# Kernel tuning notes

Hardware: AMD Instinct MI355X
Metric: run time of the kernel (lower is better)

Reference implementation:

```python
import jax, jax.numpy as jnp
import numpy as np

B, T, D = 2, 2048, 1024
H, HD = 16, 32
INNER = H * HD
FF = 4 * D
KT, KP = 3, 15


def _layernorm(x, g, b, eps=1e-5):
    mu = jnp.mean(x, axis=-1, keepdims=True)
    var = jnp.var(x, axis=-1, keepdims=True)
    return (x - mu) * jax.lax.rsqrt(var + eps) * g + b


def _causal_dwconv(x, w, b):
    # x: (b,t,d), w: (d,1,k) depthwise kernel; causal left-pad of k-1
    k = w.shape[-1]
    xc = jnp.transpose(x, (0, 2, 1))  # (b,d,t)
    xp = jnp.pad(xc, ((0, 0), (0, 0), (k - 1, 0)))
    y = jax.lax.conv_general_dilated(
        xp, w, window_strides=(1,), padding='VALID',
        feature_group_count=x.shape[-1],
        dimension_numbers=('NCH', 'OIH', 'NCH'))
    return jnp.transpose(y + b[None, :, None], (0, 2, 1))


def _causal_linear_attention(q, k, v, mask):
    # q,k,v: (b,t,h,d); mask: (b,t)
    m = mask[:, :, None, None]
    q = (jax.nn.elu(q) + 1.0) * m
    k = (jax.nn.elu(k) + 1.0) * m
    v = v * m
    kv = jnp.einsum('bthd,bthe->bthde', k, v)
    kv_prefix = jnp.cumsum(kv, axis=1)          # (b,t,h,d,e) large intermediate
    k_prefix = jnp.cumsum(k, axis=1)
    num = jnp.einsum('bthd,bthde->bthe', q, kv_prefix)
    den = jnp.sum(q * k_prefix, axis=-1, keepdims=True)
    return (num / (den + 1e-6)) * m


def setup_inputs() -> dict:
    key = jax.random.key(0)
    ks = jax.random.split(key, 10)
    w = lambda i, shape: jax.random.normal(ks[i], shape, jnp.float32) * 0.02
    return {
        'inputs': jax.random.normal(ks[0], (B, T, D), jnp.float32),
        'mask': jnp.ones((B, T), jnp.float32),
        'ln1_g': jnp.ones((D,), jnp.float32), 'ln1_b': jnp.zeros((D,), jnp.float32),
        'W_in': w(1, (D, D + 3 * INNER)), 'b_in': jnp.zeros((D + 3 * INNER,), jnp.float32),
        'W_c': w(2, (INNER, D)), 'b_c': jnp.zeros((D,), jnp.float32),
        'w_t': w(3, (D, 1, KT)), 'b_t': jnp.zeros((D,), jnp.float32),
        'w_p': w(4, (D, 1, KP)), 'b_p': jnp.zeros((D,), jnp.float32),
        'W_mix': w(5, (3 * D, D)), 'b_mix': jnp.zeros((D,), jnp.float32),
        'ln2_g': jnp.ones((D,), jnp.float32), 'ln2_b': jnp.zeros((D,), jnp.float32),
        'W1': w(6, (D, FF)), 'b1': jnp.zeros((FF,), jnp.float32),
        'W2': w(7, (FF, D)), 'b2': jnp.zeros((D,), jnp.float32),
    }


def reference(inputs, mask, ln1_g, ln1_b, W_in, b_in, W_c, b_c, w_t, b_t,
              w_p, b_p, W_mix, b_mix, ln2_g, ln2_b, W1, b1, W2, b2):
    residual = inputs
    normed = _layernorm(inputs, ln1_g, ln1_b)
    proj = normed @ W_in + b_in
    gate, q, k, v = jnp.split(proj, [D, D + INNER, D + 2 * INNER], axis=-1)
    b, t, _ = inputs.shape
    q = q.reshape(b, t, H, HD)
    k = k.reshape(b, t, H, HD)
    v = v.reshape(b, t, H, HD)
    content = _causal_linear_attention(q, k, v, mask).reshape(b, t, INNER)
    content = content @ W_c + b_c
    temporal = _causal_dwconv(normed, w_t, b_t)
    positional = _causal_dwconv(normed, w_p, b_p)
    mixed = jnp.concatenate((content, temporal, positional), axis=-1) @ W_mix + b_mix
    mask_f = mask[:, :, None]
    out = residual + jax.nn.sigmoid(gate) * mixed  # dropout=0.0 -> identity
    out = out * mask_f
    h = _layernorm(out, ln2_g, ln2_b)
    ffn = jax.nn.gelu(h @ W1 + b1, approximate=False) @ W2 + b2
    out = out + ffn
    return out * mask_f
```

## Files before the change

### kernel.cpp

```cpp
#include <hip/hip_runtime.h>
#include <math.h>

#define BB 2
#define TT 2048
#define DD 1024
#define HH 16
#define INNERD 512
#define FFD 4096
#define NPROJ 2560
#define CATD 3072
#define MROWS (BB*TT)
#define CHUNK 64
#define NCH (TT/CHUNK)
#define BH 32

typedef __bf16 bf16;
typedef __attribute__((ext_vector_type(8))) __bf16 bf16x8;
typedef __attribute__((ext_vector_type(4))) __bf16 bf16x4;
typedef __attribute__((ext_vector_type(4))) float f32x4;

struct Part4 { void* p0; void* p1; void* p2; void* p3; };

__global__ __launch_bounds__(256) void layernorm_k(
    const float* __restrict__ x, const float* __restrict__ g,
    const float* __restrict__ bta, bf16* __restrict__ y)
{
    int row = blockIdx.x, tid = threadIdx.x;
    f32x4 xv = ((const f32x4*)(x + (size_t)row * DD))[tid];
    float s = xv[0] + xv[1] + xv[2] + xv[3];
    float s2 = xv[0]*xv[0] + xv[1]*xv[1] + xv[2]*xv[2] + xv[3]*xv[3];
    #pragma unroll
    for (int off = 32; off > 0; off >>= 1) {
        s  += __shfl_xor(s,  off, 64);
        s2 += __shfl_xor(s2, off, 64);
    }
    __shared__ float rs[4], rs2[4];
    int wid = tid >> 6;
    if ((tid & 63) == 0) { rs[wid] = s; rs2[wid] = s2; }
    __syncthreads();
    s  = rs[0] + rs[1] + rs[2] + rs[3];
    s2 = rs2[0] + rs2[1] + rs2[2] + rs2[3];
    float mean = s * (1.0f / DD);
    float var  = s2 * (1.0f / DD) - mean * mean;
    float rstd = rsqrtf(var + 1e-5f);
    f32x4 gv = ((const f32x4*)g)[tid];
    f32x4 bv = ((const f32x4*)bta)[tid];
    bf16x4 o;
    #pragma unroll
    for (int q = 0; q < 4; q++)
        o[q] = (bf16)((xv[q] - mean) * rstd * gv[q] + bv[q]);
    ((bf16x4*)(y + (size_t)row * DD))[tid] = o;
}

__global__ __launch_bounds__(256) void transpose_cvt(
    const float* __restrict__ W, bf16* __restrict__ Wt, int Kd, int Nd)
{
    __shared__ float t[32][33];
    int nb = blockIdx.x * 32, kb = blockIdx.y * 32;
    int tx = threadIdx.x & 31, ty = threadIdx.x >> 5;
    #pragma unroll
    for (int r = 0; r < 32; r += 8)
        t[ty + r][tx] = W[(size_t)(kb + ty + r) * Nd + nb + tx];
    __syncthreads();
    #pragma unroll
    for (int r = 0; r < 32; r += 8)
        Wt[(size_t)(nb + ty + r) * Kd + kb + tx] = (bf16)t[tx][ty + r];
}

template<int EPI>
__global__ __launch_bounds__(256, 4) void gemm_mfma(
    const bf16* __restrict__ A,  int lda,
    const bf16* __restrict__ Bt, int ldb,
    const float* __restrict__ bias,
    bf16* __restrict__ Cb, int ldc,
    int K, Part4 part)
{
    __shared__ bf16 As[128 * 64];
    __shared__ bf16 Bs[128 * 64];
    const int tid  = threadIdx.x;
    const int wave = tid >> 6, lane = tid & 63;
    const int m0 = blockIdx.y * 128, n0 = blockIdx.x * 128;
    const int koff = blockIdx.z * K;
    A  += koff;
    Bt += koff;
    const int wr = wave >> 1, wc = wave & 1;
    const int lrow = lane >> 2;
    const int lcol = (lane & 3) * 8;
    const int fm = lane & 15;
    const int fk = (lane >> 4) * 8;

    f32x4 acc[4][4];
    #pragma unroll
    for (int i = 0; i < 4; i++)
        #pragma unroll
        for (int j = 0; j < 4; j++)
            acc[i][j] = (f32x4){0.f, 0.f, 0.f, 0.f};

    for (int k0 = 0; k0 < K; k0 += 64) {
        #pragma unroll
        for (int r = 0; r < 4; r++) {
            int c  = r * 4 + wave;
            int rc = c >> 1, kh = c & 1;
            const bf16* ga = A  + (size_t)(m0 + rc * 16 + lrow) * lda + k0 + kh * 32 + lcol;
            const bf16* gb = Bt + (size_t)(n0 + rc * 16 + lrow) * ldb + k0 + kh * 32 + lcol;
            __builtin_amdgcn_global_load_lds(
                (const __attribute__((address_space(1))) void*)ga,
                (__attribute__((address_space(3))) void*)(As + c * 512), 16, 0, 0);
            __builtin_amdgcn_global_load_lds(
                (const __attribute__((address_space(1))) void*)gb,
                (__attribute__((address_space(3))) void*)(Bs + c * 512), 16, 0, 0);
        }
        __syncthreads();
        #pragma unroll
        for (int ks = 0; ks < 2; ks++) {
            bf16x8 af[4], bfv[4];
            #pragma unroll
            for (int i = 0; i < 4; i++)
                af[i] = *(const bf16x8*)(As + (wr * 4 + i) * 1024 + ks * 512 + fm * 32 + fk);
            #pragma unroll
            for (int j = 0; j < 4; j++)
                bfv[j] = *(const bf16x8*)(Bs + (wc * 4 + j) * 1024 + ks * 512 + fm * 32 + fk);
            #pragma unroll
            for (int i = 0; i < 4; i++)
                #pragma unroll
                for (int j = 0; j < 4; j++)
                    acc[i][j] = __builtin_amdgcn_mfma_f32_16x16x32_bf16(
                        af[i], bfv[j], acc[i][j], 0, 0, 0);
        }
        __syncthreads();
    }

    void* psel = nullptr;
    if constexpr (EPI == 4 || EPI == 5) {
        int z = blockIdx.z;
        psel = (z == 0) ? part.p0 : (z == 1) ? part.p1 : (z == 2) ? part.p2 : part.p3;
    }

    #pragma unroll
    for (int i = 0; i < 4; i++) {
        int mbase = m0 + wr * 64 + i * 16 + (lane >> 4) * 4;
        #pragma unroll
        for (int j = 0; j < 4; j++) {
            int col = n0 + wc * 64 + j * 16 + (lane & 15);
            float bv = 0.f;
            if constexpr (EPI == 0 || EPI == 1) bv = bias[col];
            #pragma unroll
            for (int r = 0; r < 4; r++) {
                int row = mbase + r;
                float v = acc[i][j][r] + bv;
                if constexpr (EPI == 0) {
                    Cb[(size_t)row * ldc + col] = (bf16)v;
                } else if constexpr (EPI == 1) {
                    float z2 = v * (1.5957691f + 0.07135502f * v * v);
                    v = v / (1.0f + __expf(-z2));
                    Cb[(size_t)row * ldc + col] = (bf16)v;
                } else if constexpr (EPI == 4) {
                    ((bf16*)psel)[(size_t)row * DD + col] = (bf16)v;
                } else {
                    ((float*)psel)[(size_t)row * DD + col] = v;
                }
            }
        }
    }
}

__global__ __launch_bounds__(256) void epi_wc(
    const float* __restrict__ P0, const float* __restrict__ P1,
    const float* __restrict__ bias, bf16* __restrict__ cat)
{
    int id = blockIdx.x * 256 + threadIdx.x;
    int row = id >> 8, cg = id & 255;
    f32x4 s0 = ((const f32x4*)P0)[id];
    f32x4 s1 = ((const f32x4*)P1)[id];
    f32x4 b  = ((const f32x4*)bias)[cg];
    bf16x4 o;
    #pragma unroll
    for (int q = 0; q < 4; q++) o[q] = (bf16)(s0[q] + s1[q] + b[q]);
    *(bf16x4*)(cat + (size_t)row * CATD + cg * 4) = o;
}

__global__ __launch_bounds__(256) void epi_mix_ln2(
    const bf16* __restrict__ P0, const bf16* __restrict__ P1,
    const bf16* __restrict__ P2, const float* __restrict__ bias,
    const bf16* __restrict__ proj, const float* __restrict__ res,
    const float* __restrict__ mask,
    const float* __restrict__ g2, const float* __restrict__ b2v,
    float* __restrict__ out1, bf16* __restrict__ hbuf)
{
    int row = blockIdx.x, tid = threadIdx.x;
    float m = mask[row];
    size_t off = (size_t)row * DD + tid * 4;
    bf16x4 s0 = *(const bf16x4*)(P0 + off);
    bf16x4 s1 = *(const bf16x4*)(P1 + off);
    bf16x4 s2v = *(const bf16x4*)(P2 + off);
    f32x4 bv = ((const f32x4*)bias)[tid];
    bf16x4 g4 = *(const bf16x4*)(proj + (size_t)row * NPROJ + tid * 4);
    f32x4 rv = ((const f32x4*)(res + (size_t)row * DD))[tid];
    f32x4 v;
    #pragma unroll
    for (int q = 0; q < 4; q++) {
        float sg = 1.0f / (1.0f + __expf(-(float)g4[q]));
        float sv = (float)s0[q] + (float)s1[q] + (float)s2v[q] + bv[q];
        v[q] = (rv[q] + sg * sv) * m;
    }
    ((f32x4*)(out1 + (size_t)row * DD))[tid] = v;
    float s = v[0] + v[1] + v[2] + v[3];
    float s2 = v[0]*v[0] + v[1]*v[1] + v[2]*v[2] + v[3]*v[3];
    #pragma unroll
    for (int off2 = 32; off2 > 0; off2 >>= 1) {
        s  += __shfl_xor(s,  off2, 64);
        s2 += __shfl_xor(s2, off2, 64);
    }
    __shared__ float rs[4], rs2[4];
    int wid = tid >> 6;
    if ((tid & 63) == 0) { rs[wid] = s; rs2[wid] = s2; }
    __syncthreads();
    s  = rs[0] + rs[1] + rs[2] + rs[3];
    s2 = rs2[0] + rs2[1] + rs2[2] + rs2[3];
    float mean = s * (1.0f / DD);
    float var  = s2 * (1.0f / DD) - mean * mean;
    float rstd = rsqrtf(var + 1e-5f);
    f32x4 gg = ((const f32x4*)g2)[tid];
    f32x4 bb = ((const f32x4*)b2v)[tid];
    bf16x4 h;
    #pragma unroll
    for (int q = 0; q < 4; q++)
        h[q] = (bf16)((v[q] - mean) * rstd * gg[q] + bb[q]);
    ((bf16x4*)(hbuf + (size_t)row * DD))[tid] = h;
}

__global__ __launch_bounds__(256) void epi_w2(
    float* __restrict__ d_out, const float* __restrict__ out1,
    const bf16* __restrict__ P0, const bf16* __restrict__ P1,
    const bf16* __restrict__ P2, const bf16* __restrict__ P3,
    const float* __restrict__ bias, const float* __restrict__ mask)
{
    int id = blockIdx.x * 256 + threadIdx.x;
    int row = id >> 8;
    float m = mask[row];
    bf16x4 a0 = ((const bf16x4*)P0)[id];
    bf16x4 a1 = ((const bf16x4*)P1)[id];
    bf16x4 a2 = ((const bf16x4*)P2)[id];
    bf16x4 a3 = ((const bf16x4*)P3)[id];
    f32x4 r = ((const f32x4*)out1)[id];
    f32x4 b = ((const f32x4*)bias)[id & 255];
    f32x4 o;
    #pragma unroll
    for (int q = 0; q < 4; q++) {
        float sv = (float)a0[q] + (float)a1[q] + (float)a2[q] + (float)a3[q];
        o[q] = (r[q] + sv + b[q]) * m;
    }
    ((f32x4*)d_out)[id] = o;
}

__global__ __launch_bounds__(256) void dwconv_fused(
    const bf16* __restrict__ x,
    const float* __restrict__ w_t, const float* __restrict__ b_t,
    const float* __restrict__ w_p, const float* __restrict__ b_p,
    bf16* __restrict__ cat)
{
    int id = blockIdx.x * 256 + threadIdx.x;
    int cg = id & 127, rp = id >> 7;
    int c0 = cg * 8;
    int row0 = rp * 2;
    int t0 = row0 & (TT - 1);
    bf16x8 xw[16];
    #pragma unroll
    for (int j = 0; j < 16; j++) {
        int t = t0 - 14 + j;
        if (t >= 0)
            xw[j] = *(const bf16x8*)(x + (size_t)(row0 - 14 + j) * DD + c0);
        else
            #pragma unroll
            for (int q = 0; q < 8; q++) xw[j][q] = (bf16)0.f;
    }
    float y15[2][8], y3[2][8];
    #pragma unroll
    for (int q = 0; q < 8; q++) {
        float bp = b_p[c0 + q], bt = b_t[c0 + q];
        y15[0][q] = bp; y15[1][q] = bp;
        y3[0][q] = bt;  y3[1][q] = bt;
    }
    #pragma unroll
    for (int i = 0; i < 15; i++) {
        float wp[8];
        #pragma unroll
        for (int q = 0; q < 8; q++) wp[q] = w_p[(c0 + q) * 15 + i];
        #pragma unroll
        for (int rr = 0; rr < 2; rr++)
            #pragma unroll
            for (int q = 0; q < 8; q++)
                y15[rr][q] = fmaf(wp[q], (float)xw[rr + i][q], y15[rr][q]);
    }
    #pragma unroll
    for (int i = 0; i < 3; i++) {
        float wt[8];
        #pragma unroll
        for (int q = 0; q < 8; q++) wt[q] = w_t[(c0 + q) * 3 + i];
        #pragma unroll
        for (int rr = 0; rr < 2; rr++)
            #pragma unroll
            for (int q = 0; q < 8; q++)
                y3[rr][q] = fmaf(wt[q], (float)xw[rr + 12 + i][q], y3[rr][q]);
    }
    #pragma unroll
    for (int rr = 0; rr < 2; rr++) {
        bf16x8 o3, o15;
        #pragma unroll
        for (int q = 0; q < 8; q++) { o3[q] = (bf16)y3[rr][q]; o15[q] = (bf16)y15[rr][q]; }
        *(bf16x8*)(cat + (size_t)(row0 + rr) * CATD + DD + c0)     = o3;
        *(bf16x8*)(cat + (size_t)(row0 + rr) * CATD + 2 * DD + c0) = o15;
    }
}

__device__ __forceinline__ float phi_f(float x) {
    return x > 0.f ? x + 1.f : __expf(x);
}

__global__ __launch_bounds__(64) void attn_sums(
    const bf16* __restrict__ proj, const float* __restrict__ mask,
    float* __restrict__ kvsum, float* __restrict__ kssum)
{
    int blk = blockIdx.x;
    int c  = blk & (NCH - 1);
    int bh = blk >> 5;
    int b  = bh >> 4, hh = bh & (HH - 1);
    int lane = threadIdx.x;
    __shared__ float ks[CHUNK][32], vs[CHUNK][32];
    int row0 = b * TT + c * CHUNK;
    {
        int row = row0 + lane;
        float m = mask[row];
        const bf16* kp = proj + (size_t)row * NPROJ + DD + INNERD + hh * 32;
        const bf16* vp = kp + INNERD;
        #pragma unroll
        for (int s = 0; s < 4; s++) {
            bf16x8 k8 = *(const bf16x8*)(kp + s * 8);
            bf16x8 v8 = *(const bf16x8*)(vp + s * 8);
            #pragma unroll
            for (int q = 0; q < 8; q++) {
                ks[lane][s * 8 + q] = phi_f((float)k8[q]) * m;
                vs[lane][s * 8 + q] = (float)v8[q] * m;
            }
        }
    }
    __syncthreads();
    int e = lane & 31, d0 = (lane >> 5) * 16;
    float kv[16], ksl[16];
    #pragma unroll
    for (int j = 0; j < 16; j++) { kv[j] = 0.f; ksl[j] = 0.f; }
    for (int t = 0; t < CHUNK; t++) {
        float ve = vs[t][e];
        f32x4 kr[4];
        #pragma unroll
        for (int s = 0; s < 4; s++) kr[s] = *(const f32x4*)&ks[t][d0 + s * 4];
        #pragma unroll
        for (int j = 0; j < 16; j++) {
            float kval = kr[j >> 2][j & 3];
            kv[j] = fmaf(kval, ve, kv[j]);
            ksl[j] += kval;
        }
    }
    size_t base = (size_t)blk * 1024;
    #pragma unroll
    for (int j = 0; j < 16; j++)
        kvsum[base + (size_t)(d0 + j) * 32 + e] = kv[j];
    if (e == 0) {
        #pragma unroll
        for (int j = 0; j < 16; j++)
            kssum[blk * 32 + d0 + j] = ksl[j];
    }
}

__global__ __launch_bounds__(256) void attn_prefix(
    const float* __restrict__ kvsum, const float* __restrict__ kssum,
    float* __restrict__ kvpref, float* __restrict__ kspref)
{
    int bh = blockIdx.x;
    int tid = threadIdx.x;
    float run[4] = {0.f, 0.f, 0.f, 0.f};
    for (int c = 0; c < NCH; c++) {
        size_t base = (size_t)(bh * NCH + c) * 1024 + tid * 4;
        #pragma unroll
        for (int q = 0; q < 4; q++) {
            kvpref[base + q] = run[q];
            run[q] += kvsum[base + q];
        }
    }
    if (tid < 32) {
        float r = 0.f;
        for (int c = 0; c < NCH; c++) {
            kspref[(bh * NCH + c) * 32 + tid] = r;
            r += kssum[(bh * NCH + c) * 32 + tid];
        }
    }
}

__global__ __launch_bounds__(64) void attn_scan(
    const bf16* __restrict__ proj, const float* __restrict__ mask,
    const float* __restrict__ kvpref, const float* __restrict__ kspref,
    bf16* __restrict__ attn_out)
{
    int blk = blockIdx.x;
    int c  = blk & (NCH - 1);
    int bh = blk >> 5;
    int b  = bh >> 4, hh = bh & (HH - 1);
    int lane = threadIdx.x;
    __shared__ float qs[CHUNK][32], ks[CHUNK][32], vs[CHUNK][32];
    __shared__ float ms[CHUNK];
    int row0 = b * TT + c * CHUNK;
    {
        int row = row0 + lane;
        float m = mask[row];
        ms[lane] = m;
        const bf16* qp = proj + (size_t)row * NPROJ + DD + hh * 32;
        const bf16* kp = qp + INNERD;
        const bf16* vp = kp + INNERD;
        #pragma unroll
        for (int s = 0; s < 4; s++) {
            bf16x8 q8 = *(const bf16x8*)(qp + s * 8);
            bf16x8 k8 = *(const bf16x8*)(kp + s * 8);
            bf16x8 v8 = *(const bf16x8*)(vp + s * 8);
            #pragma unroll
            for (int q = 0; q < 8; q++) {
                qs[lane][s * 8 + q] = phi_f((float)q8[q]) * m;
                ks[lane][s * 8 + q] = phi_f((float)k8[q]) * m;
                vs[lane][s * 8 + q] = (float)v8[q] * m;
            }
        }
    }
    int e = lane & 31, d0 = (lane >> 5) * 16;
    float kv[16], ksl[16];
    size_t base = (size_t)blk * 1024;
    #pragma unroll
    for (int j = 0; j < 16; j++) kv[j] = kvpref[base + (size_t)(d0 + j) * 32 + e];
    #pragma unroll
    for (int j = 0; j < 16; j++) ksl[j] = kspref[blk * 32 + d0 + j];
    __syncthreads();
    for (int t = 0; t < CHUNK; t++) {
        float ve = vs[t][e];
        f32x4 kr[4], qr[4];
        #pragma unroll
        for (int s = 0; s < 4; s++) kr[s] = *(const f32x4*)&ks[t][d0 + s * 4];
        #pragma unroll
        for (int s = 0; s < 4; s++) qr[s] = *(const f32x4*)&qs[t][d0 + s * 4];
        float num0 = 0.f, num1 = 0.f, den0 = 0.f, den1 = 0.f;
        #pragma unroll
        for (int j = 0; j < 16; j++) {
            float kval = kr[j >> 2][j & 3], qval = qr[j >> 2][j & 3];
            kv[j]  = fmaf(kval, ve, kv[j]);
            ksl[j] += kval;
            if (j & 1) { num1 = fmaf(qval, kv[j], num1); den1 = fmaf(qval, ksl[j], den1); }
            else       { num0 = fmaf(qval, kv[j], num0); den0 = fmaf(qval, ksl[j], den0); }
        }
        float num = num0 + num1, den = den0 + den1;
        num += __shfl_xor(num, 32, 64);
        den += __shfl_xor(den, 32, 64);
        if (lane < 32)
            attn_out[(size_t)(row0 + t) * INNERD + hh * 32 + e] =
                (bf16)(num / (den + 1e-6f) * ms[t]);
    }
}

extern "C" void kernel_launch(void* const* d_in, const int* in_sizes, int n_in,
                              void* d_out, int out_size, void* d_ws, size_t ws_size,
                              hipStream_t stream)
{
    const float* inputs = (const float*)d_in[0];
    const float* mask   = (const float*)d_in[1];
    const float* ln1_g  = (const float*)d_in[2];
    const float* ln1_b  = (const float*)d_in[3];
    const float* W_in   = (const float*)d_in[4];
    const float* b_in   = (const float*)d_in[5];
    const float* W_c    = (const float*)d_in[6];
    const float* b_c    = (const float*)d_in[7];
    const float* w_t    = (const float*)d_in[8];
    const float* b_t    = (const float*)d_in[9];
    const float* w_p    = (const float*)d_in[10];
    const float* b_p    = (const float*)d_in[11];
    const float* W_mix  = (const float*)d_in[12];
    const float* b_mix  = (const float*)d_in[13];
    const float* ln2_g  = (const float*)d_in[14];
    const float* ln2_b  = (const float*)d_in[15];
    const float* W1     = (const float*)d_in[16];
    const float* b1     = (const float*)d_in[17];
    const float* W2     = (const float*)d_in[18];
    const float* b2     = (const float*)d_in[19];
    float* out = (float*)d_out;

    char* p = (char*)d_ws;
    bf16* normed = (bf16*)p;  p += (size_t)MROWS * DD * 2;
    bf16* proj   = (bf16*)p;  p += (size_t)MROWS * NPROJ * 2;
    bf16* attnb  = (bf16*)p;  p += (size_t)MROWS * INNERD * 2;
    bf16* cat    = (bf16*)p;  p += (size_t)MROWS * CATD * 2;
    float* out1  = (float*)p; p += (size_t)MROWS * DD * 4;
    bf16* hbuf   = (bf16*)p;  p += (size_t)MROWS * DD * 2;
    bf16* wt_in  = (bf16*)p;  p += (size_t)NPROJ * DD * 2;
    bf16* wt_c   = (bf16*)p;  p += (size_t)DD * INNERD * 2;
    bf16* wt_mix = (bf16*)p;  p += (size_t)DD * CATD * 2;
    bf16* wt1    = (bf16*)p;  p += (size_t)FFD * DD * 2;
    bf16* wt2    = (bf16*)p;  p += (size_t)DD * FFD * 2;
    bf16* ffn1   = (bf16*)d_ws;
    float* kvsum = out1;
    float* kvpref= kvsum  + (size_t)BH * NCH * 1024;
    float* kssum = kvpref + (size_t)BH * NCH * 1024;
    float* kspref= kssum  + (size_t)BH * NCH * 32;
    float* c_p0  = (float*)d_out;
    float* c_p1  = out1;
    bf16*  m_p0  = (bf16*)d_out;
    bf16*  m_p1  = (bf16*)d_out + (size_t)MROWS * DD;
    bf16*  m_p2  = hbuf;
    bf16*  w2_p0 = cat;
    bf16*  w2_p1 = cat + (size_t)MROWS * DD;
    bf16*  w2_p2 = cat + (size_t)MROWS * DD * 2;
    bf16*  w2_p3 = hbuf;

    transpose_cvt<<<dim3(NPROJ/32, DD/32),   256, 0, stream>>>(W_in,  wt_in,  DD,     NPROJ);
    transpose_cvt<<<dim3(DD/32,    INNERD/32),256, 0, stream>>>(W_c,   wt_c,   INNERD, DD);
    transpose_cvt<<<dim3(DD/32,    CATD/32), 256, 0, stream>>>(W_mix, wt_mix, CATD,   DD);
    transpose_cvt<<<dim3(FFD/32,   DD/32),   256, 0, stream>>>(W1,    wt1,    DD,     FFD);
    transpose_cvt<<<dim3(DD/32,    FFD/32),  256, 0, stream>>>(W2,    wt2,    FFD,    DD);

    layernorm_k<<<MROWS, 256, 0, stream>>>(inputs, ln1_g, ln1_b, normed);
    gemm_mfma<0><<<dim3(NPROJ/128, MROWS/128), 256, 0, stream>>>(
        normed, DD, wt_in, DD, b_in, proj, NPROJ, DD, Part4{});
    attn_sums  <<<BH * NCH, 64, 0, stream>>>(proj, mask, kvsum, kssum);
    attn_prefix<<<BH, 256, 0, stream>>>(kvsum, kssum, kvpref, kspref);
    attn_scan  <<<BH * NCH, 64, 0, stream>>>(proj, mask, kvpref, kspref, attnb);
    dwconv_fused<<<(MROWS/2) * 128 / 256, 256, 0, stream>>>(normed, w_t, b_t, w_p, b_p, cat);
    gemm_mfma<5><<<dim3(DD/128, MROWS/128, 2), 256, 0, stream>>>(
        attnb, INNERD, wt_c, INNERD, nullptr, nullptr, DD, INNERD / 2,
        Part4{c_p0, c_p1, nullptr, nullptr});
    epi_wc<<<MROWS * DD / 4 / 256, 256, 0, stream>>>(c_p0, c_p1, b_c, cat);
    gemm_mfma<4><<<dim3(DD/128, MROWS/128, 3), 256, 0, stream>>>(
        cat, CATD, wt_mix, CATD, nullptr, nullptr, DD, CATD / 3,
        Part4{m_p0, m_p1, m_p2, nullptr});
    epi_mix_ln2<<<MROWS, 256, 0, stream>>>(m_p0, m_p1, m_p2, b_mix, proj, inputs,
                                           mask, ln2_g, ln2_b, out1, hbuf);
    gemm_mfma<1><<<dim3(FFD/128, MROWS/128), 256, 0, stream>>>(
        hbuf, DD, wt1, DD, b1, ffn1, FFD, DD, Part4{});
    gemm_mfma<4><<<dim3(DD/128, MROWS/128, 4), 256, 0, stream>>>(
        ffn1, FFD, wt2, FFD, nullptr, nullptr, DD, FFD / 4,
        Part4{w2_p0, w2_p1, w2_p2, w2_p3});
    epi_w2<<<MROWS * DD / 4 / 256, 256, 0, stream>>>(out, out1, w2_p0, w2_p1,
                                                     w2_p2, w2_p3, b2, mask);
}
```

Baseline: 426.2 us.

## Fuse prep and mid kernels, swap GEMM grid order, store W_c partials in bf16

Merges layernorm and the five weight transpose/convert launches into one prep kernel, and merges the depthwise convs with the attention chunk-sum stage into one mid kernel that packs two attention chunks per 256-thread block. It also swaps the GEMM grid so blockIdx.x walks M tiles instead of N tiles, changing tile scheduling order and cache reuse. The split-K partials of the W_c GEMM are now written as bf16 instead of fp32, which halves that traffic but adds rounding error. The intent is fewer launches and less memory traffic. In the mid kernel, half the threads of each attention block exit immediately, and the shared-memory sync in the attention stage was removed on the assumption that each wave owns its own buffers.

```diff
diff --git a/kernel.cpp b/kernel.cpp
--- a/kernel.cpp
+++ b/kernel.cpp
@@ -21,43 +21,55 @@
 
 struct Part4 { void* p0; void* p1; void* p2; void* p3; };
 
-__global__ __launch_bounds__(256) void layernorm_k(
-    const float* __restrict__ x, const float* __restrict__ g,
-    const float* __restrict__ bta, bf16* __restrict__ y)
-{
-    int row = blockIdx.x, tid = threadIdx.x;
-    f32x4 xv = ((const f32x4*)(x + (size_t)row * DD))[tid];
-    float s = xv[0] + xv[1] + xv[2] + xv[3];
-    float s2 = xv[0]*xv[0] + xv[1]*xv[1] + xv[2]*xv[2] + xv[3]*xv[3];
-    #pragma unroll
-    for (int off = 32; off > 0; off >>= 1) {
-        s  += __shfl_xor(s,  off, 64);
-        s2 += __shfl_xor(s2, off, 64);
-    }
-    __shared__ float rs[4], rs2[4];
-    int wid = tid >> 6;
-    if ((tid & 63) == 0) { rs[wid] = s; rs2[wid] = s2; }
-    __syncthreads();
-    s  = rs[0] + rs[1] + rs[2] + rs[3];
-    s2 = rs2[0] + rs2[1] + rs2[2] + rs2[3];
-    float mean = s * (1.0f / DD);
-    float var  = s2 * (1.0f / DD) - mean * mean;
-    float rstd = rsqrtf(var + 1e-5f);
-    f32x4 gv = ((const f32x4*)g)[tid];
-    f32x4 bv = ((const f32x4*)bta)[tid];
-    bf16x4 o;
-    #pragma unroll
-    for (int q = 0; q < 4; q++)
-        o[q] = (bf16)((xv[q] - mean) * rstd * gv[q] + bv[q]);
-    ((bf16x4*)(y + (size_t)row * DD))[tid] = o;
-}
-
-__global__ __launch_bounds__(256) void transpose_cvt(
-    const float* __restrict__ W, bf16* __restrict__ Wt, int Kd, int Nd)
-{
+__global__ __launch_bounds__(256) void prep_fused(
+    const float* __restrict__ inputs, const float* __restrict__ ln1_g,
+    const float* __restrict__ ln1_b, bf16* __restrict__ normed,
+    const float* __restrict__ W_in,  bf16* __restrict__ wt_in,
+    const float* __restrict__ W_c,   bf16* __restrict__ wt_c,
+    const float* __restrict__ W_mix, bf16* __restrict__ wt_mix,
+    const float* __restrict__ W1,    bf16* __restrict__ wt1,
+    const float* __restrict__ W2,    bf16* __restrict__ wt2)
+{
+    int blk = blockIdx.x, tid = threadIdx.x;
+    if (blk < MROWS) {
+        int row = blk;
+        f32x4 xv = ((const f32x4*)(inputs + (size_t)row * DD))[tid];
+        float s = xv[0] + xv[1] + xv[2] + xv[3];
+        float s2 = xv[0]*xv[0] + xv[1]*xv[1] + xv[2]*xv[2] + xv[3]*xv[3];
+        #pragma unroll
+        for (int off = 32; off > 0; off >>= 1) {
+            s  += __shfl_xor(s,  off, 64);
+            s2 += __shfl_xor(s2, off, 64);
+        }
+        __shared__ float rs[4], rs2[4];
+        int wid = tid >> 6;
+        if ((tid & 63) == 0) { rs[wid] = s; rs2[wid] = s2; }
+        __syncthreads();
+        s  = rs[0] + rs[1] + rs[2] + rs[3];
+        s2 = rs2[0] + rs2[1] + rs2[2] + rs2[3];
+        float mean = s * (1.0f / DD);
+        float var  = s2 * (1.0f / DD) - mean * mean;
+        float rstd = rsqrtf(var + 1e-5f);
+        f32x4 gv = ((const f32x4*)ln1_g)[tid];
+        f32x4 bv = ((const f32x4*)ln1_b)[tid];
+        bf16x4 o;
+        #pragma unroll
+        for (int q = 0; q < 4; q++)
+            o[q] = (bf16)((xv[q] - mean) * rstd * gv[q] + bv[q]);
+        ((bf16x4*)(normed + (size_t)row * DD))[tid] = o;
+        return;
+    }
+    int tb = blk - MROWS;
+    const float* W; bf16* Wt; int Kd, Nd;
+    if      (tb < 2560)  {             W = W_in;  Wt = wt_in;  Kd = 1024; Nd = 2560; }
+    else if (tb < 3072)  { tb -= 2560; W = W_c;   Wt = wt_c;   Kd = 512;  Nd = 1024; }
+    else if (tb < 6144)  { tb -= 3072; W = W_mix; Wt = wt_mix; Kd = 3072; Nd = 1024; }
+    else if (tb < 10240) { tb -= 6144; W = W1;    Wt = wt1;    Kd = 1024; Nd = 4096; }
+    else                 { tb -= 10240;W = W2;    Wt = wt2;    Kd = 4096; Nd = 1024; }
+    int ntx = Nd >> 5;
+    int nb = (tb % ntx) * 32, kb = (tb / ntx) * 32;
     __shared__ float t[32][33];
-    int nb = blockIdx.x * 32, kb = blockIdx.y * 32;
-    int tx = threadIdx.x & 31, ty = threadIdx.x >> 5;
+    int tx = tid & 31, ty = tid >> 5;
     #pragma unroll
     for (int r = 0; r < 32; r += 8)
         t[ty + r][tx] = W[(size_t)(kb + ty + r) * Nd + nb + tx];
@@ -79,7 +91,7 @@
     __shared__ bf16 Bs[128 * 64];
     const int tid  = threadIdx.x;
     const int wave = tid >> 6, lane = tid & 63;
-    const int m0 = blockIdx.y * 128, n0 = blockIdx.x * 128;
+    const int m0 = blockIdx.x * 128, n0 = blockIdx.y * 128;
     const int koff = blockIdx.z * K;
     A  += koff;
     Bt += koff;
@@ -131,7 +143,7 @@
     }
 
     void* psel = nullptr;
-    if constexpr (EPI == 4 || EPI == 5) {
+    if constexpr (EPI == 4) {
         int z = blockIdx.z;
         psel = (z == 0) ? part.p0 : (z == 1) ? part.p1 : (z == 2) ? part.p2 : part.p3;
     }
@@ -154,10 +166,8 @@
                     float z2 = v * (1.5957691f + 0.07135502f * v * v);
                     v = v / (1.0f + __expf(-z2));
                     Cb[(size_t)row * ldc + col] = (bf16)v;
-                } else if constexpr (EPI == 4) {
+                } else {
                     ((bf16*)psel)[(size_t)row * DD + col] = (bf16)v;
-                } else {
-                    ((float*)psel)[(size_t)row * DD + col] = v;
                 }
             }
         }
@@ -165,17 +175,17 @@
 }
 
 __global__ __launch_bounds__(256) void epi_wc(
-    const float* __restrict__ P0, const float* __restrict__ P1,
+    const bf16* __restrict__ P0, const bf16* __restrict__ P1,
     const float* __restrict__ bias, bf16* __restrict__ cat)
 {
     int id = blockIdx.x * 256 + threadIdx.x;
     int row = id >> 8, cg = id & 255;
-    f32x4 s0 = ((const f32x4*)P0)[id];
-    f32x4 s1 = ((const f32x4*)P1)[id];
+    bf16x4 s0 = ((const bf16x4*)P0)[id];
+    bf16x4 s1 = ((const bf16x4*)P1)[id];
     f32x4 b  = ((const f32x4*)bias)[cg];
     bf16x4 o;
     #pragma unroll
-    for (int q = 0; q < 4; q++) o[q] = (bf16)(s0[q] + s1[q] + b[q]);
+    for (int q = 0; q < 4; q++) o[q] = (bf16)((float)s0[q] + (float)s1[q] + b[q]);
     *(bf16x4*)(cat + (size_t)row * CATD + cg * 4) = o;
 }
 
@@ -253,80 +263,84 @@
     ((f32x4*)d_out)[id] = o;
 }
 
-__global__ __launch_bounds__(256) void dwconv_fused(
+__device__ __forceinline__ float phi_f(float x) {
+    return x > 0.f ? x + 1.f : __expf(x);
+}
+
+__global__ __launch_bounds__(256) void mid_fused(
     const bf16* __restrict__ x,
     const float* __restrict__ w_t, const float* __restrict__ b_t,
     const float* __restrict__ w_p, const float* __restrict__ b_p,
-    bf16* __restrict__ cat)
-{
-    int id = blockIdx.x * 256 + threadIdx.x;
-    int cg = id & 127, rp = id >> 7;
-    int c0 = cg * 8;
-    int row0 = rp * 2;
-    int t0 = row0 & (TT - 1);
-    bf16x8 xw[16];
-    #pragma unroll
-    for (int j = 0; j < 16; j++) {
-        int t = t0 - 14 + j;
-        if (t >= 0)
-            xw[j] = *(const bf16x8*)(x + (size_t)(row0 - 14 + j) * DD + c0);
-        else
-            #pragma unroll
-            for (int q = 0; q < 8; q++) xw[j][q] = (bf16)0.f;
-    }
-    float y15[2][8], y3[2][8];
-    #pragma unroll
-    for (int q = 0; q < 8; q++) {
-        float bp = b_p[c0 + q], bt = b_t[c0 + q];
-        y15[0][q] = bp; y15[1][q] = bp;
-        y3[0][q] = bt;  y3[1][q] = bt;
-    }
-    #pragma unroll
-    for (int i = 0; i < 15; i++) {
-        float wp[8];
-        #pragma unroll
-        for (int q = 0; q < 8; q++) wp[q] = w_p[(c0 + q) * 15 + i];
-        #pragma unroll
-        for (int rr = 0; rr < 2; rr++)
-            #pragma unroll
-            for (int q = 0; q < 8; q++)
-                y15[rr][q] = fmaf(wp[q], (float)xw[rr + i][q], y15[rr][q]);
-    }
-    #pragma unroll
-    for (int i = 0; i < 3; i++) {
-        float wt[8];
-        #pragma unroll
-        for (int q = 0; q < 8; q++) wt[q] = w_t[(c0 + q) * 3 + i];
-        #pragma unroll
-        for (int rr = 0; rr < 2; rr++)
-            #pragma unroll
-            for (int q = 0; q < 8; q++)
-                y3[rr][q] = fmaf(wt[q], (float)xw[rr + 12 + i][q], y3[rr][q]);
-    }
-    #pragma unroll
-    for (int rr = 0; rr < 2; rr++) {
-        bf16x8 o3, o15;
-        #pragma unroll
-        for (int q = 0; q < 8; q++) { o3[q] = (bf16)y3[rr][q]; o15[q] = (bf16)y15[rr][q]; }
-        *(bf16x8*)(cat + (size_t)(row0 + rr) * CATD + DD + c0)     = o3;
-        *(bf16x8*)(cat + (size_t)(row0 + rr) * CATD + 2 * DD + c0) = o15;
-    }
-}
-
-__device__ __forceinline__ float phi_f(float x) {
-    return x > 0.f ? x + 1.f : __expf(x);
-}
-
-__global__ __launch_bounds__(64) void attn_sums(
+    bf16* __restrict__ cat,
     const bf16* __restrict__ proj, const float* __restrict__ mask,
     float* __restrict__ kvsum, float* __restrict__ kssum)
 {
-    int blk = blockIdx.x;
-    int c  = blk & (NCH - 1);
-    int bh = blk >> 5;
+    __shared__ float s_ks[2][CHUNK][32], s_vs[2][CHUNK][32];
+    int blk = blockIdx.x, tid = threadIdx.x;
+    if (blk < 1024) {
+        int id = blk * 256 + tid;
+        int cg = id & 127, rp = id >> 7;
+        int c0 = cg * 8;
+        int row0 = rp * 2;
+        int t0 = row0 & (TT - 1);
+        bf16x8 xw[16];
+        #pragma unroll
+        for (int j = 0; j < 16; j++) {
+            int t = t0 - 14 + j;
+            if (t >= 0)
+                xw[j] = *(const bf16x8*)(x + (size_t)(row0 - 14 + j) * DD + c0);
+            else
+                #pragma unroll
+                for (int q = 0; q < 8; q++) xw[j][q] = (bf16)0.f;
+        }
+        float y15[2][8], y3[2][8];
+        #pragma unroll
+        for (int q = 0; q < 8; q++) {
+            float bp = b_p[c0 + q], bt = b_t[c0 + q];
+            y15[0][q] = bp; y15[1][q] = bp;
+            y3[0][q] = bt;  y3[1][q] = bt;
+        }
+        #pragma unroll
+        for (int i = 0; i < 15; i++) {
+            float wp[8];
+            #pragma unroll
+            for (int q = 0; q < 8; q++) wp[q] = w_p[(c0 + q) * 15 + i];
+            #pragma unroll
+            for (int rr = 0; rr < 2; rr++)
+                #pragma unroll
+                for (int q = 0; q < 8; q++)
+                    y15[rr][q] = fmaf(wp[q], (float)xw[rr + i][q], y15[rr][q]);
+        }
+        #pragma unroll
+        for (int i = 0; i < 3; i++) {
+            float wt[8];
+            #pragma unroll
+            for (int q = 0; q < 8; q++) wt[q] = w_t[(c0 + q) * 3 + i];
+            #pragma unroll
+            for (int rr = 0; rr < 2; rr++)
+                #pragma unroll
+                for (int q = 0; q < 8; q++)
+                    y3[rr][q] = fmaf(wt[q], (float)xw[rr + 12 + i][q], y3[rr][q]);
+        }
+        #pragma unroll
+        for (int rr = 0; rr < 2; rr++) {
+            bf16x8 o3, o15;
+            #pragma unroll
+            for (int q = 0; q < 8; q++) { o3[q] = (bf16)y3[rr][q]; o15[q] = (bf16)y15[rr][q]; }
+            *(bf16x8*)(cat + (size_t)(row0 + rr) * CATD + DD + c0)     = o3;
+            *(bf16x8*)(cat + (size_t)(row0 + rr) * CATD + 2 * DD + c0) = o15;
+        }
+        return;
+    }
+    int w = tid >> 6;
+    if (w >= 2) return;
+    int lane = tid & 63;
+    int ci = (blk - 1024) * 2 + w;
+    int c  = ci & (NCH - 1);
+    int bh = ci >> 5;
     int b  = bh >> 4, hh = bh & (HH - 1);
-    int lane = threadIdx.x;
-    __shared__ float ks[CHUNK][32], vs[CHUNK][32];
+    float (*ks)[32] = s_ks[w];
+    float (*vs)[32] = s_vs[w];
     int row0 = b * TT + c * CHUNK;
     {
         int row = row0 + lane;
@@ -344,7 +358,6 @@
             }
         }
     }
-    __syncthreads();
     int e = lane & 31, d0 = (lane >> 5) * 16;
     float kv[16], ksl[16];
     #pragma unroll
@@ -361,14 +374,14 @@
             ksl[j] += kval;
         }
     }
-    size_t base = (size_t)blk * 1024;
+    size_t base = (size_t)ci * 1024;
     #pragma unroll
     for (int j = 0; j < 16; j++)
         kvsum[base + (size_t)(d0 + j) * 32 + e] = kv[j];
     if (e == 0) {
         #pragma unroll
         for (int j = 0; j < 16; j++)
-            kssum[blk * 32 + d0 + j] = ksl[j];
+            kssum[ci * 32 + d0 + j] = ksl[j];
     }
 }
 
@@ -505,8 +518,8 @@
     float* kvpref= kvsum  + (size_t)BH * NCH * 1024;
     float* kssum = kvpref + (size_t)BH * NCH * 1024;
     float* kspref= kssum  + (size_t)BH * NCH * 32;
-    float* c_p0  = (float*)d_out;
-    float* c_p1  = out1;
+    bf16*  c_p0  = (bf16*)d_out;
+    bf16*  c_p1  = (bf16*)out1;
     bf16*  m_p0  = (bf16*)d_out;
     bf16*  m_p1  = (bf16*)d_out + (size_t)MROWS * DD;
     bf16*  m_p2  = hbuf;
@@ -515,31 +528,27 @@
     bf16*  w2_p2 = cat + (size_t)MROWS * DD * 2;
     bf16*  w2_p3 = hbuf;
 
-    transpose_cvt<<<dim3(NPROJ/32, DD/32),   256, 0, stream>>>(W_in,  wt_in,  DD,     NPROJ);
-    transpose_cvt<<<dim3(DD/32,    INNERD/32),256, 0, stream>>>(W_c,   wt_c,   INNERD, DD);
-    transpose_cvt<<<dim3(DD/32,    CATD/32), 256, 0, stream>>>(W_mix, wt_mix, CATD,   DD);
-    transpose_cvt<<<dim3(FFD/32,   DD/32),   256, 0, stream>>>(W1,    wt1,    DD,     FFD);
-    transpose_cvt<<<dim3(DD/32,    FFD/32),  256, 0, stream>>>(W2,    wt2,    FFD,    DD);
-
-    layernorm_k<<<MROWS, 256, 0, stream>>>(inputs, ln1_g, ln1_b, normed);
-    gemm_mfma<0><<<dim3(NPROJ/128, MROWS/128), 256, 0, stream>>>(
+    prep_fused<<<MROWS + 14336, 256, 0, stream>>>(
+        inputs, ln1_g, ln1_b, normed,
+        W_in, wt_in, W_c, wt_c, W_mix, wt_mix, W1, wt1, W2, wt2);
+    gemm_mfma<0><<<dim3(MROWS/128, NPROJ/128), 256, 0, stream>>>(
         normed, DD, wt_in, DD, b_in, proj, NPROJ, DD, Part4{});
-    attn_sums  <<<BH * NCH, 64, 0, stream>>>(proj, mask, kvsum, kssum);
+    mid_fused<<<1024 + 512, 256, 0, stream>>>(
+        normed, w_t, b_t, w_p, b_p, cat, proj, mask, kvsum, kssum);
     attn_prefix<<<BH, 256, 0, stream>>>(kvsum, kssum, kvpref, kspref);
     attn_scan  <<<BH * NCH, 64, 0, stream>>>(proj, mask, kvpref, kspref, attnb);
-    dwconv_fused<<<(MROWS/2) * 128 / 256, 256, 0, stream>>>(normed, w_t, b_t, w_p, b_p, cat);
-    gemm_mfma<5><<<dim3(DD/128, MROWS/128, 2), 256, 0, stream>>>(
+    gemm_mfma<4><<<dim3(MROWS/128, DD/128, 2), 256, 0, stream>>>(
         attnb, INNERD, wt_c, INNERD, nullptr, nullptr, DD, INNERD / 2,
         Part4{c_p0, c_p1, nullptr, nullptr});
     epi_wc<<<MROWS * DD / 4 / 256, 256, 0, stream>>>(c_p0, c_p1, b_c, cat);
-    gemm_mfma<4><<<dim3(DD/128, MROWS/128, 3), 256, 0, stream>>>(
+    gemm_mfma<4><<<dim3(MROWS/128, DD/128, 3), 256, 0, stream>>>(
         cat, CATD, wt_mix, CATD, nullptr, nullptr, DD, CATD / 3,
         Part4{m_p0, m_p1, m_p2, nullptr});
     epi_mix_ln2<<<MROWS, 256, 0, stream>>>(m_p0, m_p1, m_p2, b_mix, proj, inputs,
                                            mask, ln2_g, ln2_b, out1, hbuf);
-    gemm_mfma<1><<<dim3(FFD/128, MROWS/128), 256, 0, stream>>>(
+    gemm_mfma<1><<<dim3(MROWS/128, FFD/128), 256, 0, stream>>>(
         hbuf, DD, wt1, DD, b1, ffn1, FFD, DD, Part4{});
-    gemm_mfma<4><<<dim3(DD/128, MROWS/128, 4), 256, 0, stream>>>(
+    gemm_mfma<4><<<dim3(MROWS/128, DD/128, 4), 256, 0, stream>>>(
         ffn1, FFD, wt2, FFD, nullptr, nullptr, DD, FFD / 4,
         Part4{w2_p0, w2_p1, w2_p2, w2_p3});
     epi_w2<<<MROWS * DD / 4 / 256, 256, 0, stream>>>(out, out1, w2_p0, w2_p1,
```

New measurement: 396.3 us. -7.0%, faster.
